# Kernel tuning notes

Hardware: AMD Instinct MI355X
Metric: run time of the kernel (lower is better)

Reference implementation:

```python
import jax, jax.numpy as jnp
import numpy as np

D_IN = 1024
D_OUT = 1024
NUM_HEADS = 16
D_HEAD = D_OUT // NUM_HEADS


def setup_inputs() -> dict:
    key = jax.random.key(0)
    ks = jax.random.split(key, 6)
    s = 0.02
    return {
        "x": jax.random.normal(ks[0], (2, 2048, D_IN), dtype=jnp.float32),
        "W_q": jax.random.normal(ks[1], (D_IN, D_OUT), dtype=jnp.float32) * s,
        "W_k": jax.random.normal(ks[2], (D_IN, D_OUT), dtype=jnp.float32) * s,
        "W_v": jax.random.normal(ks[3], (D_IN, D_OUT), dtype=jnp.float32) * s,
        "W_o": jax.random.normal(ks[4], (D_OUT, D_OUT), dtype=jnp.float32) * s,
        "b_o": jax.random.normal(ks[5], (D_OUT,), dtype=jnp.float32) * s,
    }


def reference(x, W_q, W_k, W_v, W_o, b_o):
    B, T, _ = x.shape
    # qkv projections (no bias), split heads -> [B, H, T, d_head]
    def split_heads(t):
        return t.reshape(B, T, NUM_HEADS, D_HEAD).transpose(0, 2, 1, 3)
    q = split_heads(x @ W_q)
    k = split_heads(x @ W_k)
    v = split_heads(x @ W_v)
    # full causal scores [B, H, T, T]
    scores = jnp.einsum("bhqd,bhkd->bhqk", q, k)
    causal = jnp.triu(jnp.ones((T, T), dtype=bool), k=1)
    scores = jnp.where(causal, -jnp.inf, scores)
    attn = jax.nn.softmax(scores / np.sqrt(D_HEAD).astype(np.float32), axis=-1)
    # dropout rate is 0.0 -> identity
    ctx = jnp.einsum("bhqk,bhkd->bhqd", attn, v)
    ctx = ctx.transpose(0, 2, 1, 3).reshape(B, T, D_OUT)
    return ctx @ W_o + b_o
```

## Files before the change

kernel.cpp:

```cpp
#include <hip/hip_runtime.h>
#include <hip/hip_bf16.h>
#include <cstdint>

#define SEQ_T 2048
#define DMODEL 1024
#define NHEAD 16
#define DHEAD 64

typedef __attribute__((ext_vector_type(8))) __bf16 bf16x8;
typedef __attribute__((ext_vector_type(4))) float floatx4;

static __device__ __forceinline__ uint16_t f2bf(float f) {
    union { float f; uint32_t u; } v; v.f = f;
    uint32_t r = v.u + 0x7FFFu + ((v.u >> 16) & 1u);
    return (uint16_t)(r >> 16);
}

__global__ void mha_cvt(const float* __restrict__ x, uint16_t* __restrict__ xb,
                        const float* __restrict__ W0, const float* __restrict__ W1,
                        const float* __restrict__ W2, const float* __restrict__ W3,
                        uint16_t* __restrict__ T0, uint16_t* __restrict__ T1,
                        uint16_t* __restrict__ T2, uint16_t* __restrict__ T3) {
    if (blockIdx.z == 4) {
        int base = (blockIdx.y * 16 + blockIdx.x) * 256 + threadIdx.x;
#pragma unroll
        for (int i = 0; i < 16; ++i) {
            int idx = base + i * 65536;
            float4 f = ((const float4*)x)[idx];
            union { uint16_t u[4]; uint64_t v; } o;
            o.u[0] = f2bf(f.x); o.u[1] = f2bf(f.y); o.u[2] = f2bf(f.z); o.u[3] = f2bf(f.w);
            ((uint64_t*)xb)[idx] = o.v;
        }
        return;
    }
    const float* W; uint16_t* Tt; float sc;
    switch (blockIdx.z) {
        case 0: W = W0; Tt = T0; sc = 0.125f * 1.44269504089f; break;
        case 1: W = W1; Tt = T1; sc = 1.f; break;
        case 2: W = W2; Tt = T2; sc = 1.f; break;
        default: W = W3; Tt = T3; sc = 1.f; break;
    }
    __shared__ float tile[64][65];
    const int c  = threadIdx.x & 63;
    const int r0 = threadIdx.x >> 6;
    const int R0 = blockIdx.y * 64, C0 = blockIdx.x * 64;
#pragma unroll
    for (int rr = 0; rr < 16; ++rr) {
        int r = r0 + rr * 4;
        tile[r][c] = W[(size_t)(R0 + r) * DMODEL + C0 + c];
    }
    __syncthreads();
#pragma unroll
    for (int rr = 0; rr < 16; ++rr) {
        int r = r0 + rr * 4;
        Tt[(size_t)(C0 + r) * DMODEL + R0 + c] = f2bf(tile[c][r] * sc);
    }
}

template<int MODE>
__device__ __forceinline__ void gemm_bk64_body(
    const uint16_t* __restrict__ A, const uint16_t* __restrict__ Bt,
    uint16_t* __restrict__ outB) {
    const int K = DMODEL, N = DMODEL;
    extern __shared__ char smem[];
    uint16_t* As = (uint16_t*)smem;
    uint16_t* Bs = (uint16_t*)(smem + 8192);
    const int tid  = threadIdx.x;
    const int wave = tid >> 6;
    const int lane = tid & 63;
    const int m0 = blockIdx.y * 64;
    const int n0 = blockIdx.x * 128;
    const int lr   = lane & 15;
    const int quad = lane >> 4;

    floatx4 acc[4][2];
#pragma unroll
    for (int i = 0; i < 4; ++i)
#pragma unroll
        for (int j = 0; j < 2; ++j) acc[i][j] = (floatx4)0.0f;

    for (int k0 = 0; k0 < K; k0 += 64) {
#pragma unroll
        for (int i = 0; i < 2; ++i) {
            int c = i * 256 + tid;
            int r = c >> 3, s = (c & 7) ^ (r & 7);
            const uint16_t* g = A + (size_t)(m0 + r) * K + k0 + s * 8;
            __builtin_amdgcn_global_load_lds((const __attribute__((address_space(1))) void*)g,
                                             (__attribute__((address_space(3))) void*)(As + (size_t)c * 8), 16, 0, 0);
        }
#pragma unroll
        for (int i = 0; i < 4; ++i) {
            int c = i * 256 + tid;
            int r = c >> 3, s = (c & 7) ^ (r & 7);
            const uint16_t* g = Bt + (size_t)(n0 + r) * K + k0 + s * 8;
            __builtin_amdgcn_global_load_lds((const __attribute__((address_space(1))) void*)g,
                                             (__attribute__((address_space(3))) void*)(Bs + (size_t)c * 8), 16, 0, 0);
        }
        __syncthreads();
#pragma unroll
        for (int ks = 0; ks < 2; ++ks) {
            bf16x8 af[4], bfr[2];
#pragma unroll
            for (int mi = 0; mi < 4; ++mi) {
                int row = mi * 16 + lr;
                af[mi] = *(const bf16x8*)&As[row * 64 + (((ks * 4 + quad) ^ (row & 7)) << 3)];
            }
#pragma unroll
            for (int ni = 0; ni < 2; ++ni) {
                int row = wave * 32 + ni * 16 + lr;
                bfr[ni] = *(const bf16x8*)&Bs[row * 64 + (((ks * 4 + quad) ^ (row & 7)) << 3)];
            }
#pragma unroll
            for (int mi = 0; mi < 4; ++mi)
#pragma unroll
                for (int ni = 0; ni < 2; ++ni)
                    acc[mi][ni] = __builtin_amdgcn_mfma_f32_16x16x32_bf16(af[mi], bfr[ni], acc[mi][ni], 0, 0, 0);
        }
        __syncthreads();
    }
    if constexpr (MODE == 1) {
        uint16_t* Ct = (uint16_t*)smem;
        const int bb = m0 >> 11, t0 = m0 & 2047;
#pragma unroll
        for (int mi = 0; mi < 4; ++mi)
#pragma unroll
            for (int ni = 0; ni < 2; ++ni) {
                int cl = wave * 32 + ni * 16 + lr;
                int tl = mi * 16 + quad * 4;
                int tls = tl ^ ((cl & 3) << 4);
                union { uint16_t u[4]; uint64_t v8; } pk;
#pragma unroll
                for (int r = 0; r < 4; ++r) pk.u[r] = f2bf(acc[mi][ni][r]);
                *(uint64_t*)&Ct[cl * 72 + tls] = pk.v8;
            }
        __syncthreads();
#pragma unroll
        for (int k = 0; k < 4; ++k) {
            int c = k * 256 + tid;
            int cl = c >> 3, off = (c & 7) * 8;
            int offs = off ^ ((cl & 3) << 4);
            uint4 v = *(const uint4*)&Ct[cl * 72 + offs];
            *(uint4*)&outB[((size_t)(bb * 1024 + n0 + cl)) * 2048 + t0 + off] = v;
        }
    } else {
#pragma unroll
        for (int mi = 0; mi < 4; ++mi)
#pragma unroll
            for (int ni = 0; ni < 2; ++ni) {
                int col = n0 + wave * 32 + ni * 16 + lr;
#pragma unroll
                for (int r = 0; r < 4; ++r) {
                    int row = m0 + mi * 16 + quad * 4 + r;
                    outB[(size_t)row * N + col] = f2bf(acc[mi][ni][r]);
                }
            }
    }
}

__global__ __launch_bounds__(256) void mha_gemm_qkv(
    const uint16_t* __restrict__ A,
    const uint16_t* __restrict__ Wq, const uint16_t* __restrict__ Wk, const uint16_t* __restrict__ Wv,
    uint16_t* __restrict__ Q, uint16_t* __restrict__ K, uint16_t* __restrict__ Vt) {
    switch (blockIdx.z) {
        case 0:  gemm_bk64_body<0>(A, Wq, Q);  break;
        case 1:  gemm_bk64_body<0>(A, Wk, K);  break;
        default: gemm_bk64_body<1>(A, Wv, Vt); break;
    }
}

__global__ __launch_bounds__(512) void mha_gemm_out(
    const uint16_t* __restrict__ A, const uint16_t* __restrict__ Wot,
    float* __restrict__ out, const float* __restrict__ bias) {
    const int K = DMODEL, N = DMODEL;
    extern __shared__ char smem[];
    uint16_t* As = (uint16_t*)smem;
    uint16_t* Bs = (uint16_t*)(smem + 8192);
    const int tid  = threadIdx.x;
    const int wave = tid >> 6;
    const int lane = tid & 63;
    const int m0 = blockIdx.y * 64;
    const int n0 = blockIdx.x * 128;
    const int lr   = lane & 15;
    const int quad = lane >> 4;
    const int wm = wave >> 2, wn = wave & 3;

    floatx4 acc[2][2];
#pragma unroll
    for (int i = 0; i < 2; ++i)
#pragma unroll
        for (int j = 0; j < 2; ++j) acc[i][j] = (floatx4)0.0f;

    for (int k0 = 0; k0 < K; k0 += 64) {
        {
            int c = tid;
            int r = c >> 3, s = (c & 7) ^ (r & 7);
            const uint16_t* g = A + (size_t)(m0 + r) * K + k0 + s * 8;
            __builtin_amdgcn_global_load_lds((const __attribute__((address_space(1))) void*)g,
                                             (__attribute__((address_space(3))) void*)(As + (size_t)c * 8), 16, 0, 0);
        }
#pragma unroll
        for (int i = 0; i < 2; ++i) {
            int c = i * 512 + tid;
            int r = c >> 3, s = (c & 7) ^ (r & 7);
            const uint16_t* g = Wot + (size_t)(n0 + r) * K + k0 + s * 8;
            __builtin_amdgcn_global_load_lds((const __attribute__((address_space(1))) void*)g,
                                             (__attribute__((address_space(3))) void*)(Bs + (size_t)c * 8), 16, 0, 0);
        }
        __syncthreads();
#pragma unroll
        for (int ks = 0; ks < 2; ++ks) {
            bf16x8 af[2], bfr[2];
#pragma unroll
            for (int mi = 0; mi < 2; ++mi) {
                int row = wm * 32 + mi * 16 + lr;
                af[mi] = *(const bf16x8*)&As[row * 64 + (((ks * 4 + quad) ^ (row & 7)) << 3)];
            }
#pragma unroll
            for (int ni = 0; ni < 2; ++ni) {
                int row = wn * 32 + ni * 16 + lr;
                bfr[ni] = *(const bf16x8*)&Bs[row * 64 + (((ks * 4 + quad) ^ (row & 7)) << 3)];
            }
#pragma unroll
            for (int mi = 0; mi < 2; ++mi)
#pragma unroll
                for (int ni = 0; ni < 2; ++ni)
                    acc[mi][ni] = __builtin_amdgcn_mfma_f32_16x16x32_bf16(af[mi], bfr[ni], acc[mi][ni], 0, 0, 0);
        }
        __syncthreads();
    }
#pragma unroll
    for (int mi = 0; mi < 2; ++mi)
#pragma unroll
        for (int ni = 0; ni < 2; ++ni) {
            int col = n0 + wn * 32 + ni * 16 + lr;
            float bv = bias[col];
#pragma unroll
            for (int r = 0; r < 4; ++r) {
                int row = m0 + wm * 32 + mi * 16 + quad * 4 + r;
                out[(size_t)row * N + col] = acc[mi][ni][r] + bv;
            }
        }
}

__global__ __launch_bounds__(512, 4) void mha_attn_mfma(
    const uint16_t* __restrict__ Q, const uint16_t* __restrict__ K,
    const uint16_t* __restrict__ Vt, uint16_t* __restrict__ ctx) {
    __shared__ alignas(16) uint16_t KsB[2][128 * 64];
    __shared__ alignas(16) uint16_t VsB[2][64 * 128];
    __shared__ alignas(16) uint16_t Pb[64 * 128];

    const int tid  = threadIdx.x;
    const int wave = tid >> 6;
    const int lane = tid & 63;
    const int lr   = lane & 15;
    const int quad = lane >> 4;
    const int qw   = wave & 3;
    const int kvh  = wave >> 2;
    const int h  = blockIdx.x;
    const int p  = blockIdx.y;
    const int b  = blockIdx.z;
    const int jH = 31 - p, jL = p;
    const int TH = (33 - p) >> 1;

    const uint16_t* kg[2];
    const uint16_t* vg[2];
#pragma unroll
    for (int i = 0; i < 2; ++i) {
        int c  = i * 512 + tid;
        int rk = c >> 3, sk = (c & 7) ^ (rk & 7);
        kg[i] = K + ((size_t)(b * SEQ_T) + rk) * DMODEL + h * DHEAD + sk * 8;
        int rv = c >> 4, hv = (c >> 3) & 1, sv = (c & 7) ^ (rv & 7);
        vg[i] = Vt + ((size_t)(b * 1024 + h * DHEAD + rv)) * 2048 + hv * 64 + sv * 8;
    }

    int wrow = jH * 64 + qw * 16;
    bf16x8 qf0, qf1;
    {
        const size_t qb = ((size_t)(b * SEQ_T) + wrow + lr) * DMODEL + h * DHEAD;
        qf0 = *(const bf16x8*)(Q + qb + quad * 8);
        qf1 = *(const bf16x8*)(Q + qb + 32 + quad * 8);
    }
    bf16x8 ones;
#pragma unroll
    for (int i = 0; i < 8; ++i) ones[i] = (__bf16)1.0f;

    floatx4 o[4];
#pragma unroll
    for (int nt = 0; nt < 4; ++nt) o[nt] = (floatx4)0.0f;
    floatx4 lacc = (floatx4)0.0f;

    auto stage = [&](int kv0, int buf) {
#pragma unroll
        for (int i = 0; i < 2; ++i) {
            int c = i * 512 + tid;
            __builtin_amdgcn_global_load_lds(
                (const __attribute__((address_space(1))) void*)(kg[i] + (size_t)kv0 * DMODEL),
                (__attribute__((address_space(3))) void*)(&KsB[buf][c * 8]), 16, 0, 0);
            __builtin_amdgcn_global_load_lds(
                (const __attribute__((address_space(1))) void*)(vg[i] + kv0),
                (__attribute__((address_space(3))) void*)(&VsB[buf][c * 8]), 16, 0, 0);
        }
    };

    auto combine_store = [&](int cur) {
        __syncthreads();
        float* Pbf = (float*)Pb;
        float* Lf  = (float*)&VsB[cur][0];
        if (kvh == 1) {
#pragma unroll
            for (int nt = 0; nt < 4; ++nt)
#pragma unroll
                for (int r = 0; r < 4; ++r)
                    Pbf[(qw * 16 + quad * 4 + r) * 64 + ((nt ^ quad) * 16 + lr)] = o[nt][r];
            if (lr == 0) {
#pragma unroll
                for (int r = 0; r < 4; ++r) Lf[qw * 16 + quad * 4 + r] = lacc[r];
            }
        }
        __syncthreads();
        if (kvh == 0) {
            float linv[4];
#pragma unroll
            for (int r = 0; r < 4; ++r)
                linv[r] = 1.f / (lacc[r] + Lf[qw * 16 + quad * 4 + r]);
#pragma unroll
            for (int nt = 0; nt < 4; ++nt)
#pragma unroll
                for (int r = 0; r < 4; ++r) {
                    float ov = o[nt][r] + Pbf[(qw * 16 + quad * 4 + r) * 64 + ((nt ^ quad) * 16 + lr)];
                    size_t addr = ((size_t)(b * SEQ_T) + wrow + quad * 4 + r) * DMODEL + h * DHEAD + nt * 16 + lr;
                    ctx[addr] = f2bf(ov * linv[r]);
                }
        }
    };

    stage(0, 0);
    __syncthreads();

    for (int t = 0; t < 17; ++t) {
        const int cur = t & 1;
        const int kv0 = (t < TH ? t : t - TH) * 128;
        if (t + 1 < 17) {
            const int tn = t + 1;
            stage((tn < TH ? tn : tn - TH) * 128, tn & 1);
        }

        const int kvb = kv0 + kvh * 64;
        floatx4 s[4];
#pragma unroll
        for (int nt = 0; nt < 4; ++nt) {
            s[nt] = (floatx4)0.0f;
            int krow = kvh * 64 + nt * 16 + lr;
#pragma unroll
            for (int ks = 0; ks < 2; ++ks) {
                bf16x8 kf = *(const bf16x8*)&KsB[cur][krow * 64 + (((ks * 4 + quad) ^ (lr & 7)) * 8)];
                s[nt] = __builtin_amdgcn_mfma_f32_16x16x32_bf16(ks ? qf1 : qf0, kf, s[nt], 0, 0, 0);
            }
        }
        if (kvb + 63 > wrow) {
#pragma unroll
            for (int nt = 0; nt < 4; ++nt) {
                int kcol = kvb + nt * 16 + lr;
#pragma unroll
                for (int r = 0; r < 4; ++r) {
                    int qrow = wrow + quad * 4 + r;
                    if (kcol > qrow) s[nt][r] = -3e38f;
                }
            }
        }
#pragma unroll
        for (int nt = 0; nt < 4; ++nt)
#pragma unroll
            for (int r = 0; r < 4; ++r) {
                float pe = __builtin_amdgcn_exp2f(s[nt][r]);
                int row = qw * 16 + quad * 4 + r;
                int cc  = kvh * 8 + ((nt * 2 + (lr >> 3)) ^ (row & 7));
                Pb[row * 128 + cc * 8 + (lr & 7)] = (uint16_t)(__float_as_uint(pe) >> 16);
            }
#pragma unroll
        for (int ks = 0; ks < 2; ++ks) {
            int prow = qw * 16 + lr;
            bf16x8 pfr = *(const bf16x8*)&Pb[prow * 128 + ((kvh * 8 + ((ks * 4 + quad) ^ (prow & 7))) * 8)];
            lacc = __builtin_amdgcn_mfma_f32_16x16x32_bf16(pfr, ones, lacc, 0, 0, 0);
#pragma unroll
            for (int nt = 0; nt < 4; ++nt) {
                int vrow = nt * 16 + lr;
                bf16x8 vf = *(const bf16x8*)&VsB[cur][vrow * 128 + ((kvh * 8 + ((ks * 4 + quad) ^ (lr & 7))) * 8)];
                o[nt] = __builtin_amdgcn_mfma_f32_16x16x32_bf16(pfr, vf, o[nt], 0, 0, 0);
            }
        }
        if (t == TH - 1) {
            combine_store(cur);
            wrow = jL * 64 + qw * 16;
            const size_t qb = ((size_t)(b * SEQ_T) + wrow + lr) * DMODEL + h * DHEAD;
            qf0 = *(const bf16x8*)(Q + qb + quad * 8);
            qf1 = *(const bf16x8*)(Q + qb + 32 + quad * 8);
#pragma unroll
            for (int nt = 0; nt < 4; ++nt) o[nt] = (floatx4)0.0f;
            lacc = (floatx4)0.0f;
        }
        if (t + 1 < 17) __syncthreads();
    }
    combine_store(0);
}

extern "C" void kernel_launch(void* const* d_in, const int* in_sizes, int n_in,
                              void* d_out, int out_size, void* d_ws, size_t ws_size,
                              hipStream_t stream) {
    const float* x  = (const float*)d_in[0];
    const float* Wq = (const float*)d_in[1];
    const float* Wk = (const float*)d_in[2];
    const float* Wv = (const float*)d_in[3];
    const float* Wo = (const float*)d_in[4];
    const float* bo = (const float*)d_in[5];
    float* out = (float*)d_out;

    char* ws = (char*)d_ws;
    const size_t SZ_X = (size_t)4096 * DMODEL * 2;
    const size_t SZ_W = (size_t)DMODEL * DMODEL * 2;
    size_t off = 0;
    uint16_t* xb  = (uint16_t*)(ws + off); off += SZ_X;
    uint16_t* wqt = (uint16_t*)(ws + off); off += SZ_W;
    uint16_t* wkt = (uint16_t*)(ws + off); off += SZ_W;
    uint16_t* wvt = (uint16_t*)(ws + off); off += SZ_W;
    uint16_t* wot = (uint16_t*)(ws + off); off += SZ_W;
    uint16_t* Qb  = (uint16_t*)(ws + off); off += SZ_X;
    uint16_t* Kb  = (uint16_t*)(ws + off); off += SZ_X;
    uint16_t* Vtb = (uint16_t*)(ws + off); off += SZ_X;
    uint16_t* Cb  = (uint16_t*)(ws + off); off += SZ_X;
    (void)ws_size; (void)in_sizes; (void)n_in; (void)out_size;

    mha_cvt<<<dim3(16, 16, 5), 256, 0, stream>>>(x, xb, Wq, Wk, Wv, Wo, wqt, wkt, wvt, wot);
    mha_gemm_qkv<<<dim3(8, 64, 3), 256, 24576, stream>>>(xb, wqt, wkt, wvt, Qb, Kb, Vtb);
    mha_attn_mfma<<<dim3(NHEAD, 16, 2), 512, 0, stream>>>(Qb, Kb, Vtb, Cb);
    mha_gemm_out<<<dim3(8, 64), 512, 24576, stream>>>(Cb, wot, out, bo);
}
```

Baseline: 171.1 us.

## Switch attention to 32x32x16 MFMA with register-resident P via permlane32 swap

Rewrites the attention kernel to use 32x32x16 bf16 MFMA tiles with 4 waves per block (256 threads) instead of 16x16x32 tiles with 8 waves. It computes S transposed (K as the A operand) so the exp'd probabilities can be repacked into the PV operand in registers using permlane32_swap, removing the shared-memory P round trip and the ones-MFMA row sum. Row sums are accumulated in scalar registers. The intent is fewer LDS writes and reads and fewer barriers, at the cost of more work per wave and higher register pressure.

```diff
diff --git a/kernel.cpp b/kernel.cpp
--- a/kernel.cpp
+++ b/kernel.cpp
@@ -9,11 +9,19 @@
 
 typedef __attribute__((ext_vector_type(8))) __bf16 bf16x8;
 typedef __attribute__((ext_vector_type(4))) float floatx4;
+typedef __attribute__((ext_vector_type(16))) float floatx16;
+typedef __attribute__((ext_vector_type(2))) unsigned uint32x2;
 
 static __device__ __forceinline__ uint16_t f2bf(float f) {
     union { float f; uint32_t u; } v; v.f = f;
     uint32_t r = v.u + 0x7FFFu + ((v.u >> 16) & 1u);
     return (uint16_t)(r >> 16);
+}
+
+static __device__ __forceinline__ uint32_t pack2bf(float a, float b) {
+    union { __bf16 h[2]; uint32_t u; } p;
+    p.h[0] = (__bf16)a; p.h[1] = (__bf16)b;
+    return p.u;
 }
 
 __global__ void mha_cvt(const float* __restrict__ x, uint16_t* __restrict__ xb,
@@ -242,94 +250,103 @@
         }
 }
 
-__global__ __launch_bounds__(512, 4) void mha_attn_mfma(
+__global__ __launch_bounds__(256, 4) void mha_attn_mfma(
     const uint16_t* __restrict__ Q, const uint16_t* __restrict__ K,
     const uint16_t* __restrict__ Vt, uint16_t* __restrict__ ctx) {
-    __shared__ alignas(16) uint16_t KsB[2][128 * 64];
-    __shared__ alignas(16) uint16_t VsB[2][64 * 128];
-    __shared__ alignas(16) uint16_t Pb[64 * 128];
+    __shared__ alignas(16) uint16_t Ks[2][128 * 64];
+    __shared__ alignas(16) uint16_t Vs[2][64 * 128];
 
     const int tid  = threadIdx.x;
     const int wave = tid >> 6;
     const int lane = tid & 63;
-    const int lr   = lane & 15;
-    const int quad = lane >> 4;
-    const int qw   = wave & 3;
-    const int kvh  = wave >> 2;
-    const int h  = blockIdx.x;
-    const int p  = blockIdx.y;
-    const int b  = blockIdx.z;
+    const int l31  = lane & 31;
+    const int hi   = lane >> 5;
+    const int l7   = lane & 7;
+    const int qg   = wave & 1;
+    const int kvh  = wave >> 1;
+    const int h = blockIdx.x;
+    const int p = blockIdx.y;
+    const int b = blockIdx.z;
     const int jH = 31 - p, jL = p;
-    const int TH = (33 - p) >> 1;
-
-    const uint16_t* kg[2];
-    const uint16_t* vg[2];
-#pragma unroll
-    for (int i = 0; i < 2; ++i) {
-        int c  = i * 512 + tid;
-        int rk = c >> 3, sk = (c & 7) ^ (rk & 7);
-        kg[i] = K + ((size_t)(b * SEQ_T) + rk) * DMODEL + h * DHEAD + sk * 8;
-        int rv = c >> 4, hv = (c >> 3) & 1, sv = (c & 7) ^ (rv & 7);
-        vg[i] = Vt + ((size_t)(b * 1024 + h * DHEAD + rv)) * 2048 + hv * 64 + sv * 8;
-    }
-
-    int wrow = jH * 64 + qw * 16;
-    bf16x8 qf0, qf1;
-    {
-        const size_t qb = ((size_t)(b * SEQ_T) + wrow + lr) * DMODEL + h * DHEAD;
-        qf0 = *(const bf16x8*)(Q + qb + quad * 8);
-        qf1 = *(const bf16x8*)(Q + qb + 32 + quad * 8);
-    }
-    bf16x8 ones;
-#pragma unroll
-    for (int i = 0; i < 8; ++i) ones[i] = (__bf16)1.0f;
-
-    floatx4 o[4];
-#pragma unroll
-    for (int nt = 0; nt < 4; ++nt) o[nt] = (floatx4)0.0f;
-    floatx4 lacc = (floatx4)0.0f;
+    const int TH = (jH + 2) >> 1;
+
+    const uint16_t* kg[4];
+    const uint16_t* vg[4];
+    int cch[4];
+#pragma unroll
+    for (int i = 0; i < 4; ++i) {
+        int c = i * 256 + tid; cch[i] = c;
+        int rk = c >> 3, ck = c & 7;
+        kg[i] = K + ((size_t)(b * SEQ_T) + rk) * DMODEL + h * DHEAD + (ck ^ (rk & 7)) * 8;
+        int rv = c >> 4, cv = c & 15;
+        int sv = (cv & 8) | ((cv & 7) ^ (rv & 7));
+        vg[i] = Vt + ((size_t)(b * 1024 + h * DHEAD + rv)) * 2048 + sv * 8;
+    }
+
+    int q0w = jH * 64 + qg * 32;
+    bf16x8 qf[4];
+    auto load_q = [&]() {
+        const uint16_t* qb = Q + ((size_t)(b * SEQ_T) + q0w + l31) * DMODEL + h * DHEAD;
+#pragma unroll
+        for (int f = 0; f < 4; ++f)
+            qf[f] = *(const bf16x8*)(qb + f * 16 + hi * 8);
+    };
+    load_q();
+
+    floatx16 o[2];
+#pragma unroll
+    for (int dt = 0; dt < 2; ++dt) o[dt] = (floatx16)0.0f;
+    float lac = 0.f;
 
     auto stage = [&](int kv0, int buf) {
 #pragma unroll
-        for (int i = 0; i < 2; ++i) {
-            int c = i * 512 + tid;
+        for (int i = 0; i < 4; ++i) {
             __builtin_amdgcn_global_load_lds(
                 (const __attribute__((address_space(1))) void*)(kg[i] + (size_t)kv0 * DMODEL),
-                (__attribute__((address_space(3))) void*)(&KsB[buf][c * 8]), 16, 0, 0);
+                (__attribute__((address_space(3))) void*)(&Ks[buf][cch[i] * 8]), 16, 0, 0);
             __builtin_amdgcn_global_load_lds(
                 (const __attribute__((address_space(1))) void*)(vg[i] + kv0),
-                (__attribute__((address_space(3))) void*)(&VsB[buf][c * 8]), 16, 0, 0);
+                (__attribute__((address_space(3))) void*)(&Vs[buf][cch[i] * 8]), 16, 0, 0);
         }
     };
 
+    auto halfsum = [&](float x) -> float {
+#if __has_builtin(__builtin_amdgcn_permlane32_swap)
+        uint32x2 r = __builtin_amdgcn_permlane32_swap(__float_as_uint(x), __float_as_uint(x), false, false);
+        return __uint_as_float(r.x) + __uint_as_float(r.y);
+#else
+        return x + __shfl_xor(x, 32, 64);
+#endif
+    };
+
     auto combine_store = [&](int cur) {
         __syncthreads();
-        float* Pbf = (float*)Pb;
-        float* Lf  = (float*)&VsB[cur][0];
+        float* osc = (float*)&Vs[cur][0];
+        float* lsc = (float*)&Ks[cur][0];
+        float lt = halfsum(lac);
         if (kvh == 1) {
-#pragma unroll
-            for (int nt = 0; nt < 4; ++nt)
-#pragma unroll
-                for (int r = 0; r < 4; ++r)
-                    Pbf[(qw * 16 + quad * 4 + r) * 64 + ((nt ^ quad) * 16 + lr)] = o[nt][r];
-            if (lr == 0) {
-#pragma unroll
-                for (int r = 0; r < 4; ++r) Lf[qw * 16 + quad * 4 + r] = lacc[r];
-            }
+            if (lane < 32) lsc[qg * 32 + lane] = lt;
+#pragma unroll
+            for (int dt = 0; dt < 2; ++dt)
+#pragma unroll
+                for (int r = 0; r < 16; ++r) {
+                    int row = (r & 3) + 8 * (r >> 2) + 4 * hi;
+                    osc[(qg * 32 + row) * 64 + dt * 32 + l31] = o[dt][r];
+                }
         }
         __syncthreads();
         if (kvh == 0) {
-            float linv[4];
-#pragma unroll
-            for (int r = 0; r < 4; ++r)
-                linv[r] = 1.f / (lacc[r] + Lf[qw * 16 + quad * 4 + r]);
-#pragma unroll
-            for (int nt = 0; nt < 4; ++nt)
-#pragma unroll
-                for (int r = 0; r < 4; ++r) {
-                    float ov = o[nt][r] + Pbf[(qw * 16 + quad * 4 + r) * 64 + ((nt ^ quad) * 16 + lr)];
-                    size_t addr = ((size_t)(b * SEQ_T) + wrow + quad * 4 + r) * DMODEL + h * DHEAD + nt * 16 + lr;
-                    ctx[addr] = f2bf(ov * linv[r]);
+            float ltot = lt + lsc[qg * 32 + l31];
+            if (lane < 32) lsc[64 + qg * 32 + lane] = 1.f / ltot;
+#pragma unroll
+            for (int dt = 0; dt < 2; ++dt)
+#pragma unroll
+                for (int r = 0; r < 16; ++r) {
+                    int row = (r & 3) + 8 * (r >> 2) + 4 * hi;
+                    float ov = o[dt][r] + osc[(qg * 32 + row) * 64 + dt * 32 + l31];
+                    float li = lsc[64 + qg * 32 + row];
+                    size_t addr = ((size_t)(b * SEQ_T) + q0w + row) * DMODEL + h * DHEAD + dt * 32 + l31;
+                    ctx[addr] = f2bf(ov * li);
                 }
         }
     };
@@ -341,63 +358,85 @@
         const int cur = t & 1;
         const int kv0 = (t < TH ? t : t - TH) * 128;
         if (t + 1 < 17) {
-            const int tn = t + 1;
+            int tn = t + 1;
             stage((tn < TH ? tn : tn - TH) * 128, tn & 1);
         }
-
-        const int kvb = kv0 + kvh * 64;
-        floatx4 s[4];
-#pragma unroll
-        for (int nt = 0; nt < 4; ++nt) {
-            s[nt] = (floatx4)0.0f;
-            int krow = kvh * 64 + nt * 16 + lr;
-#pragma unroll
-            for (int ks = 0; ks < 2; ++ks) {
-                bf16x8 kf = *(const bf16x8*)&KsB[cur][krow * 64 + (((ks * 4 + quad) ^ (lr & 7)) * 8)];
-                s[nt] = __builtin_amdgcn_mfma_f32_16x16x32_bf16(ks ? qf1 : qf0, kf, s[nt], 0, 0, 0);
-            }
-        }
-        if (kvb + 63 > wrow) {
-#pragma unroll
-            for (int nt = 0; nt < 4; ++nt) {
-                int kcol = kvb + nt * 16 + lr;
-#pragma unroll
-                for (int r = 0; r < 4; ++r) {
-                    int qrow = wrow + quad * 4 + r;
-                    if (kcol > qrow) s[nt][r] = -3e38f;
+#pragma unroll
+        for (int kt = 0; kt < 2; ++kt) {
+            const int kb = kv0 + kvh * 64 + kt * 32;
+            floatx16 s = (floatx16)0.0f;
+#pragma unroll
+            for (int f = 0; f < 4; ++f) {
+                bf16x8 kf = *(const bf16x8*)&Ks[cur][(kvh * 64 + kt * 32 + l31) * 64 + (((2 * f + hi) ^ l7) << 3)];
+                s = __builtin_amdgcn_mfma_f32_32x32x16_bf16(kf, qf[f], s, 0, 0, 0);
+            }
+            if (kb + 31 > q0w) {
+                int qr = q0w + l31;
+#pragma unroll
+                for (int r = 0; r < 16; ++r) {
+                    int k = kb + (r & 3) + 8 * (r >> 2) + 4 * hi;
+                    if (k > qr) s[r] = -3e38f;
                 }
             }
-        }
-#pragma unroll
-        for (int nt = 0; nt < 4; ++nt)
-#pragma unroll
-            for (int r = 0; r < 4; ++r) {
-                float pe = __builtin_amdgcn_exp2f(s[nt][r]);
-                int row = qw * 16 + quad * 4 + r;
-                int cc  = kvh * 8 + ((nt * 2 + (lr >> 3)) ^ (row & 7));
-                Pb[row * 128 + cc * 8 + (lr & 7)] = (uint16_t)(__float_as_uint(pe) >> 16);
-            }
-#pragma unroll
-        for (int ks = 0; ks < 2; ++ks) {
-            int prow = qw * 16 + lr;
-            bf16x8 pfr = *(const bf16x8*)&Pb[prow * 128 + ((kvh * 8 + ((ks * 4 + quad) ^ (prow & 7))) * 8)];
-            lacc = __builtin_amdgcn_mfma_f32_16x16x32_bf16(pfr, ones, lacc, 0, 0, 0);
-#pragma unroll
-            for (int nt = 0; nt < 4; ++nt) {
-                int vrow = nt * 16 + lr;
-                bf16x8 vf = *(const bf16x8*)&VsB[cur][vrow * 128 + ((kvh * 8 + ((ks * 4 + quad) ^ (lr & 7))) * 8)];
-                o[nt] = __builtin_amdgcn_mfma_f32_16x16x32_bf16(pfr, vf, o[nt], 0, 0, 0);
-            }
+            float se[16];
+#pragma unroll
+            for (int r = 0; r < 16; ++r) {
+                se[r] = __builtin_amdgcn_exp2f(s[r]);
+                lac += se[r];
+            }
+            uint32_t d0[2], d1[2], d2[2], d3[2];
+#pragma unroll
+            for (int i = 0; i < 2; ++i) {
+                d0[i] = pack2bf(se[2 * i],      se[2 * i + 1]);
+                d1[i] = pack2bf(se[4 + 2 * i],  se[4 + 2 * i + 1]);
+                d2[i] = pack2bf(se[8 + 2 * i],  se[8 + 2 * i + 1]);
+                d3[i] = pack2bf(se[12 + 2 * i], se[12 + 2 * i + 1]);
+            }
+            bf16x8 paf[2];
+#if __has_builtin(__builtin_amdgcn_permlane32_swap)
+            {
+                uint32x2 r0 = __builtin_amdgcn_permlane32_swap(d0[0], d1[0], false, false);
+                uint32x2 r1 = __builtin_amdgcn_permlane32_swap(d0[1], d1[1], false, false);
+                union { uint32_t u[4]; bf16x8 v; } f0;
+                f0.u[0] = r0.x; f0.u[1] = r1.x; f0.u[2] = r0.y; f0.u[3] = r1.y;
+                paf[0] = f0.v;
+                uint32x2 r2 = __builtin_amdgcn_permlane32_swap(d2[0], d3[0], false, false);
+                uint32x2 r3 = __builtin_amdgcn_permlane32_swap(d2[1], d3[1], false, false);
+                union { uint32_t u[4]; bf16x8 v; } f1;
+                f1.u[0] = r2.x; f1.u[1] = r3.x; f1.u[2] = r2.y; f1.u[3] = r3.y;
+                paf[1] = f1.v;
+            }
+#else
+            {
+                uint32_t s00 = __shfl_xor((int)d0[0], 32, 64), s01 = __shfl_xor((int)d0[1], 32, 64);
+                uint32_t s10 = __shfl_xor((int)d1[0], 32, 64), s11 = __shfl_xor((int)d1[1], 32, 64);
+                union { uint32_t u[4]; bf16x8 v; } f0;
+                f0.u[0] = hi ? s10 : d0[0]; f0.u[1] = hi ? s11 : d0[1];
+                f0.u[2] = hi ? d1[0] : s00; f0.u[3] = hi ? d1[1] : s01;
+                paf[0] = f0.v;
+                uint32_t s20 = __shfl_xor((int)d2[0], 32, 64), s21 = __shfl_xor((int)d2[1], 32, 64);
+                uint32_t s30 = __shfl_xor((int)d3[0], 32, 64), s31 = __shfl_xor((int)d3[1], 32, 64);
+                union { uint32_t u[4]; bf16x8 v; } f1;
+                f1.u[0] = hi ? s30 : d2[0]; f1.u[1] = hi ? s31 : d2[1];
+                f1.u[2] = hi ? d3[0] : s20; f1.u[3] = hi ? d3[1] : s21;
+                paf[1] = f1.v;
+            }
+#endif
+#pragma unroll
+            for (int f = 0; f < 2; ++f)
+#pragma unroll
+                for (int dt = 0; dt < 2; ++dt) {
+                    bf16x8 vf = *(const bf16x8*)&Vs[cur][(dt * 32 + l31) * 128 + ((kvh * 8 + ((kt * 4 + 2 * f + hi) ^ l7)) << 3)];
+                    o[dt] = __builtin_amdgcn_mfma_f32_32x32x16_bf16(paf[f], vf, o[dt], 0, 0, 0);
+                }
         }
         if (t == TH - 1) {
             combine_store(cur);
-            wrow = jL * 64 + qw * 16;
-            const size_t qb = ((size_t)(b * SEQ_T) + wrow + lr) * DMODEL + h * DHEAD;
-            qf0 = *(const bf16x8*)(Q + qb + quad * 8);
-            qf1 = *(const bf16x8*)(Q + qb + 32 + quad * 8);
-#pragma unroll
-            for (int nt = 0; nt < 4; ++nt) o[nt] = (floatx4)0.0f;
-            lacc = (floatx4)0.0f;
+            q0w = jL * 64 + qg * 32;
+            load_q();
+#pragma unroll
+            for (int dt = 0; dt < 2; ++dt) o[dt] = (floatx16)0.0f;
+            lac = 0.f;
         }
         if (t + 1 < 17) __syncthreads();
     }
@@ -432,6 +471,6 @@
 
     mha_cvt<<<dim3(16, 16, 5), 256, 0, stream>>>(x, xb, Wq, Wk, Wv, Wo, wqt, wkt, wvt, wot);
     mha_gemm_qkv<<<dim3(8, 64, 3), 256, 24576, stream>>>(xb, wqt, wkt, wvt, Qb, Kb, Vtb);
-    mha_attn_mfma<<<dim3(NHEAD, 16, 2), 512, 0, stream>>>(Qb, Kb, Vtb, Cb);
+    mha_attn_mfma<<<dim3(NHEAD, 16, 2), 256, 0, stream>>>(Qb, Kb, Vtb, Cb);
     mha_gemm_out<<<dim3(8, 64), 512, 24576, stream>>>(Cb, wot, out, bo);
 }
```

New measurement: 175.1 us. +2.3%, slower.
